# Performance work log

Measured on AMD Instinct MI355X. Metric: run time of the kernel, lower is better.

The kernel has to match this reference:

```python
import jax, jax.numpy as jnp
import numpy as np
import math

NUM_HEADS = 16
HEAD_DIM = 64
DIM = 1024
IO_SLOTS = 16
NEG_INF = 1.0e9


def _alibi_slopes(num_heads):
    # slopes = ratio**i for i in 1..n, ratio = 2**(-8/n)
    ratio = 2.0 ** (-8.0 / num_heads)
    return jnp.array([ratio ** i for i in range(1, num_heads + 1)], dtype=jnp.float32)


def setup_inputs() -> dict:
    key = jax.random.key(0)
    ks = jax.random.split(key, 7)
    B, S, D = 2, 2048, DIM
    x = jax.random.normal(ks[0], (B, S, D), dtype=jnp.float32)
    is_getchar = jax.random.uniform(ks[1], (B, S), dtype=jnp.float32)
    is_putchar = jax.random.uniform(ks[2], (B, S), dtype=jnp.float32)
    scale = 0.02
    wq = jax.random.normal(ks[3], (D, NUM_HEADS * HEAD_DIM), dtype=jnp.float32) * scale
    wk = jax.random.normal(ks[4], (D, NUM_HEADS * HEAD_DIM), dtype=jnp.float32) * scale
    wv = jax.random.normal(ks[5], (D, NUM_HEADS * HEAD_DIM), dtype=jnp.float32) * scale
    wo = jax.random.normal(ks[6], (NUM_HEADS * HEAD_DIM, D), dtype=jnp.float32) * scale
    return {"x": x, "is_getchar": is_getchar, "is_putchar": is_putchar,
            "wq": wq, "wk": wk, "wv": wv, "wo": wo}


def reference(x, is_getchar, is_putchar, wq, wk, wv, wo):
    B, S, D = x.shape
    H, hd = NUM_HEADS, HEAD_DIM
    io_start = D - IO_SLOTS

    q = (x @ wq).reshape(B, S, H, hd)
    k = (x @ wk).reshape(B, S, H, hd)
    v = (x @ wv).reshape(B, S, H, hd)

    # scores[b,h,i,j] = q . k / sqrt(hd)
    scores = jnp.einsum("bihd,bjhd->bhij", q, k) / math.sqrt(hd)

    # standard ALiBi bias: -slope * (i - j), causal masked
    positions = jnp.arange(S)
    dist = (positions[:, None] - positions[None, :]).astype(jnp.float32)  # [S,S] = i - j
    slopes = _alibi_slopes(H)  # [H]
    bias = -slopes[:, None, None] * dist  # [H,S,S]
    causal = jnp.triu(jnp.ones((S, S), dtype=jnp.float32), k=1)
    bias = bias - causal * NEG_INF
    scores = scores + bias[None]

    # targeted read-head bias on head 0: -slope0 * |target - j|
    read_anchor = x[..., io_start + 0]  # [B,S]
    read_offset = x[..., io_start + 1]  # [B,S]
    target = read_anchor + 1.0 + read_offset  # [B,S]
    read_bias = -slopes[0] * jnp.abs(target[..., None] - positions.astype(jnp.float32))  # [B,S,S]
    head0 = jnp.where(is_getchar[:, None, :, None] > 0.5, read_bias[:, None], scores[:, :1])
    scores = scores.at[:, :1].set(head0)

    attn = jax.nn.softmax(scores, axis=-1)
    attn_out = jnp.einsum("bhij,bjhd->bihd", attn, v).reshape(B, S, H * hd)
    output = x + attn_out @ wo

    # I/O state updates (last 16 channels)
    output = output.at[..., io_start + 1].add(is_getchar)   # read_offset += getchar
    output = output.at[..., io_start + 3].add(is_putchar)   # write_offset += putchar
    output = output.at[..., io_start + 13].set(is_putchar)  # output_ready = putchar
    return output
```

## Files before the change

kernel.cpp:

```cpp
#include <hip/hip_runtime.h>
#include <hip/hip_bf16.h>

typedef __hip_bfloat16 bf16;
typedef __attribute__((ext_vector_type(8))) short short8;
typedef __attribute__((ext_vector_type(4))) short short4v;
typedef __attribute__((ext_vector_type(4))) float f32x4;

#define MFMA16(a, b, c) __builtin_amdgcn_mfma_f32_16x16x32_bf16((a), (b), (c), 0, 0, 0)

#if __has_builtin(__builtin_amdgcn_mfma_f32_16x16x16bf16_1k)
#define MFMA_PV(a, b, c) __builtin_amdgcn_mfma_f32_16x16x16bf16_1k((a), (b), (c), 0, 0, 0)
#elif __has_builtin(__builtin_amdgcn_mfma_f32_16x16x16_bf16)
#define MFMA_PV(a, b, c) __builtin_amdgcn_mfma_f32_16x16x16_bf16((a), (b), (c), 0, 0, 0)
#else
static __device__ __forceinline__ f32x4 mfma_pv_asm(short4v a, short4v b, f32x4 c) {
    f32x4 d;
    asm volatile("v_mfma_f32_16x16x16_bf16 %0, %1, %2, %3"
                 : "=&v"(d) : "v"(a), "v"(b), "v"(c));
    return d;
}
#define MFMA_PV(a, b, c) mfma_pv_asm((a), (b), (c))
#endif

static __device__ __forceinline__ void gload_lds16(const bf16* g, bf16* l) {
    __builtin_amdgcn_global_load_lds((const __attribute__((address_space(1))) void*)g,
                                     (__attribute__((address_space(3))) void*)l, 16, 0, 0);
}

__global__ __launch_bounds__(256) void cast_x_kernel(const float* __restrict__ in,
                                                     bf16* __restrict__ out) {
    int i = (blockIdx.x * 256 + threadIdx.x) * 4;
    float4 v = *(const float4*)(in + i);
    union { bf16 h4[4]; uint2 u; } p;
    p.h4[0] = __float2bfloat16(v.x);
    p.h4[1] = __float2bfloat16(v.y);
    p.h4[2] = __float2bfloat16(v.z);
    p.h4[3] = __float2bfloat16(v.w);
    *(uint2*)(out + i) = p.u;
}

__global__ __launch_bounds__(256) void transpose_cast_kernel(
    const float* __restrict__ wq, const float* __restrict__ wk,
    const float* __restrict__ wv, const float* __restrict__ wo,
    bf16* __restrict__ WqkvT, bf16* __restrict__ WoT) {
    __shared__ bf16 tile[64][65];
    int bid = blockIdx.x;
    int mat = bid >> 8;
    int t   = bid & 255;
    int tn  = t >> 4, tk = t & 15;
    const float* src = (mat == 0) ? wq : (mat == 1) ? wk : (mat == 2) ? wv : wo;
    bf16* dst = (mat < 3) ? (WqkvT + (size_t)mat * 1024 * 1024) : WoT;
    int tx = threadIdx.x & 63, ty = threadIdx.x >> 6;
    int k0 = tk * 64, n0 = tn * 64;
#pragma unroll
    for (int p = 0; p < 16; ++p) {
        int r = p * 4 + ty;
        tile[r][tx] = __float2bfloat16(src[(size_t)(k0 + r) * 1024 + n0 + tx]);
    }
    __syncthreads();
#pragma unroll
    for (int p = 0; p < 16; ++p) {
        int r = p * 4 + ty;
        dst[(size_t)(n0 + r) * 1024 + k0 + tx] = tile[tx][r];
    }
}

__global__ __launch_bounds__(256) void gemm_qkv_kernel(
    const bf16* __restrict__ A, const bf16* __restrict__ Bt,
    bf16* __restrict__ QK, bf16* __restrict__ Vt) {
    const int K = 1024;
    int bm = blockIdx.x, bn = blockIdx.y;
    __shared__ bf16 As[128 * 32];
    __shared__ bf16 Bs[128 * 32];
    int tid = threadIdx.x;
    int lane = tid & 63, w = tid >> 6;
    int wm = (w >> 1) * 64, wn = (w & 1) * 64;
    int q4 = lane >> 4, li = lane & 15;
    int srow = tid >> 2, sc = (tid & 3) * 8;

    const bf16* Ag = A + (size_t)(bm * 128 + srow) * K + sc;
    const bf16* Bg = Bt + (size_t)(bn * 128 + srow) * K + sc;
    bf16* Asl = As + tid * 8;
    bf16* Asl2 = As + 2048 + tid * 8;
    bf16* Bsl = Bs + tid * 8;
    bf16* Bsl2 = Bs + 2048 + tid * 8;

    f32x4 acc[4][4];
#pragma unroll
    for (int mt = 0; mt < 4; ++mt)
#pragma unroll
        for (int nt = 0; nt < 4; ++nt) acc[mt][nt] = (f32x4){0.f, 0.f, 0.f, 0.f};

    for (int k0 = 0; k0 < K; k0 += 32) {
        __syncthreads();
        gload_lds16(Ag + k0, Asl);
        gload_lds16(Ag + 64 * K + k0, Asl2);
        gload_lds16(Bg + k0, Bsl);
        gload_lds16(Bg + 64 * K + k0, Bsl2);
        __syncthreads();
        short8 af[4], bfb[4];
#pragma unroll
        for (int mt = 0; mt < 4; ++mt)
            af[mt] = *(const short8*)(As + (wm + mt * 16 + li) * 32 + q4 * 8);
#pragma unroll
        for (int nt = 0; nt < 4; ++nt)
            bfb[nt] = *(const short8*)(Bs + (wn + nt * 16 + li) * 32 + q4 * 8);
#pragma unroll
        for (int mt = 0; mt < 4; ++mt)
#pragma unroll
            for (int nt = 0; nt < 4; ++nt)
                acc[mt][nt] = MFMA16(af[mt], bfb[nt], acc[mt][nt]);
    }

    int rowb = bm * 128 + wm;
    if (bn < 16) {
#pragma unroll
        for (int mt = 0; mt < 4; ++mt) {
#pragma unroll
            for (int nt = 0; nt < 4; ++nt) {
                int col = bn * 128 + wn + nt * 16 + li;
#pragma unroll
                for (int r = 0; r < 4; ++r) {
                    int row = rowb + mt * 16 + q4 * 4 + r;
                    QK[(size_t)row * 2048 + col] = __float2bfloat16(acc[mt][nt][r]);
                }
            }
        }
    } else {
#pragma unroll
        for (int mt = 0; mt < 4; ++mt) {
            int sbase = rowb + mt * 16 + q4 * 4;
            int b = sbase >> 11, s = sbase & 2047;
#pragma unroll
            for (int nt = 0; nt < 4; ++nt) {
                int n = bn * 128 + wn + nt * 16 + li - 2048;
                int h = n >> 6, d = n & 63;
                union { bf16 h4[4]; uint2 u; } pk;
#pragma unroll
                for (int r = 0; r < 4; ++r) pk.h4[r] = __float2bfloat16(acc[mt][nt][r]);
                *(uint2*)(Vt + (size_t)((b * 16 + h) * 64 + d) * 2048 + s) = pk.u;
            }
        }
    }
}

__global__ __launch_bounds__(256, 3) void attn_kernel(
    const bf16* __restrict__ QK, const bf16* __restrict__ Vt,
    const float* __restrict__ x, const float* __restrict__ gch,
    bf16* __restrict__ AO) {
    const int S = 2048;
    int idx = blockIdx.x;
    int ti, h, b;
    if (idx < 64) { h = 0; b = idx & 1; ti = idx >> 1; }
    else {
        int i2 = idx - 64;
        int row = i2 / 30;
        int j = i2 - row * 30;
        ti = 31 - row; h = 1 + (j >> 1); b = j & 1;
    }
    int i0 = ti * 64;
    int tid = threadIdx.x, lane = tid & 63, w = tid >> 6;
    int q4 = lane >> 4, li = lane & 15;

    __shared__ bf16 Ks[64 * 72];
    __shared__ bf16 Vs[64 * 72];
    __shared__ float Ored[64 * 68];
    __shared__ float lsumBuf[4][64];

    short8 qf[4][2];
#pragma unroll
    for (int it = 0; it < 4; ++it) {
        const bf16* qp = QK + (size_t)(b * S + i0 + it * 16 + li) * 2048 + h * 64 + q4 * 8;
        qf[it][0] = *(const short8*)(qp);
        qf[it][1] = *(const short8*)(qp + 32);
    }

    const float L2E = 1.4426950408889634f;
    float slope = exp2f(-0.5f * (float)(h + 1));
    float s1  = 0.125f * L2E;
    float sl1 = slope * L2E;
    const float slope0_1 = 0.70710678118654752f * L2E;

    float tgt[4]; int gcm[4];
    if (h == 0) {
#pragma unroll
        for (int it = 0; it < 4; ++it) {
            size_t ix = (size_t)(b * S + i0 + it * 16 + li);
            gcm[it] = gch[ix] > 0.5f ? 1 : 0;
            tgt[it] = x[ix * 1024 + 1008] + 1.0f + x[ix * 1024 + 1009];
        }
    } else {
#pragma unroll
        for (int it = 0; it < 4; ++it) { gcm[it] = 0; tgt[it] = 0.f; }
    }

    float lsum[4] = {0.f, 0.f, 0.f, 0.f};
    f32x4 o[4][4];
#pragma unroll
    for (int it = 0; it < 4; ++it)
#pragma unroll
        for (int dt = 0; dt < 4; ++dt) o[it][dt] = (f32x4){0.f, 0.f, 0.f, 0.f};

    int srow = tid >> 3, scv = (tid & 7) * 8;
    const bf16* Kg = QK + (size_t)(b * S + srow) * 2048 + 1024 + h * 64 + scv;
    const bf16* Vg = Vt + (size_t)((b * 16 + h) * 64 + srow) * 2048 + scv;

    int ntiles = (h == 0) ? (S / 64) : (ti + 1);
    for (int jt = 0; jt < ntiles; ++jt) {
        int j0 = jt * 64;
        uint4 kv0 = *(const uint4*)(Kg + (size_t)j0 * 2048);
        uint4 kv1 = *(const uint4*)(Kg + (size_t)(j0 + 32) * 2048);
        uint4 vv0 = *(const uint4*)(Vg + j0);
        uint4 vv1 = *(const uint4*)(Vg + (size_t)32 * 2048 + j0);
        __syncthreads();
        *(uint4*)(Ks + srow * 72 + scv) = kv0;
        *(uint4*)(Ks + (srow + 32) * 72 + scv) = kv1;
        *(uint4*)(Vs + srow * 72 + scv) = vv0;
        *(uint4*)(Vs + (srow + 32) * 72 + scv) = vv1;
        __syncthreads();

        short8 kf0 = *(const short8*)(Ks + (w * 16 + li) * 72 + q4 * 8);
        short8 kf1 = *(const short8*)(Ks + (w * 16 + li) * 72 + 32 + q4 * 8);
        f32x4 sAcc[4];
#pragma unroll
        for (int it = 0; it < 4; ++it) {
            f32x4 z = (f32x4){0.f, 0.f, 0.f, 0.f};
            z = MFMA16(kf0, qf[it][0], z);
            z = MFMA16(kf1, qf[it][1], z);
            sAcc[it] = z;
        }

        float jbase = (float)(j0 + w * 16 + q4 * 4);
        int maskable = (jt >= ti);
        short4v pf[4];
#pragma unroll
        for (int it = 0; it < 4; ++it) {
            float fi = (float)(i0 + it * 16 + li);
            float d0 = jbase - fi;
            union { bf16 hh[4]; short4v v; } pu;
#pragma unroll
            for (int r = 0; r < 4; ++r) {
                float dj = d0 + (float)r;
                float s = fmaf(sl1, dj, sAcc[it][r] * s1);
                float p;
                if (h == 0) {
                    float jj = jbase + (float)r;
                    float sg = -slope0_1 * fabsf(tgt[it] - jj);
                    s = gcm[it] ? sg : s;
                    bool msk = (!gcm[it]) && (dj > 0.f);
                    p = msk ? 0.f : exp2f(s);
                } else {
                    p = exp2f(s);
                    if (maskable && dj > 0.f) p = 0.f;
                }
                lsum[it] += p;
                pu.hh[r] = __float2bfloat16(p);
            }
            pf[it] = pu.v;
        }

#pragma unroll
        for (int dt = 0; dt < 4; ++dt) {
            short4v vf = *(const short4v*)(Vs + (dt * 16 + li) * 72 + w * 16 + q4 * 4);
#pragma unroll
            for (int it = 0; it < 4; ++it)
                o[it][dt] = MFMA_PV(pf[it], vf, o[it][dt]);
        }
    }

#pragma unroll
    for (int it = 0; it < 4; ++it) {
        lsum[it] += __shfl_xor(lsum[it], 16, 64);
        lsum[it] += __shfl_xor(lsum[it], 32, 64);
    }
    if (lane < 16) {
#pragma unroll
        for (int it = 0; it < 4; ++it) lsumBuf[w][it * 16 + lane] = lsum[it];
    }

    __syncthreads();
    if (w == 0) {
#pragma unroll
        for (int it = 0; it < 4; ++it)
#pragma unroll
            for (int dt = 0; dt < 4; ++dt)
#pragma unroll
                for (int r = 0; r < 4; ++r)
                    Ored[(it * 16 + q4 * 4 + r) * 68 + dt * 16 + li] = o[it][dt][r];
    }
    __syncthreads();
    if (w == 1) {
#pragma unroll
        for (int it = 0; it < 4; ++it)
#pragma unroll
            for (int dt = 0; dt < 4; ++dt)
#pragma unroll
                for (int r = 0; r < 4; ++r)
                    Ored[(it * 16 + q4 * 4 + r) * 68 + dt * 16 + li] += o[it][dt][r];
    }
    __syncthreads();
    if (w == 2) {
#pragma unroll
        for (int it = 0; it < 4; ++it)
#pragma unroll
            for (int dt = 0; dt < 4; ++dt)
#pragma unroll
                for (int r = 0; r < 4; ++r)
                    Ored[(it * 16 + q4 * 4 + r) * 68 + dt * 16 + li] += o[it][dt][r];
    }
    __syncthreads();
    if (w == 3) {
#pragma unroll
        for (int it = 0; it < 4; ++it)
#pragma unroll
            for (int dt = 0; dt < 4; ++dt)
#pragma unroll
                for (int r = 0; r < 4; ++r)
                    Ored[(it * 16 + q4 * 4 + r) * 68 + dt * 16 + li] += o[it][dt][r];
    }
    __syncthreads();

    int i = tid >> 2, dseg = (tid & 3) * 16;
    float ls = lsumBuf[0][i] + lsumBuf[1][i] + lsumBuf[2][i] + lsumBuf[3][i];
    float inv = 1.0f / ls;
    bf16* dst = AO + (size_t)(b * S + i0 + i) * 1024 + h * 64 + dseg;
    union { bf16 hh[16]; uint4 u[2]; } ou;
#pragma unroll
    for (int c = 0; c < 16; ++c)
        ou.hh[c] = __float2bfloat16(Ored[i * 68 + dseg + c] * inv);
    *(uint4*)(dst) = ou.u[0];
    *(uint4*)(dst + 8) = ou.u[1];
}

__global__ __launch_bounds__(256) void gemm_out_kernel(
    const bf16* __restrict__ A, const bf16* __restrict__ Bt,
    const float* __restrict__ x, float* __restrict__ out) {
    const int K = 1024;
    int bm = blockIdx.x, bn = blockIdx.y;
    __shared__ bf16 As[128 * 32];
    __shared__ bf16 Bs[128 * 32];
    int tid = threadIdx.x;
    int lane = tid & 63, w = tid >> 6;
    int wm = (w >> 1) * 64, wn = (w & 1) * 64;
    int q4 = lane >> 4, li = lane & 15;
    int srow = tid >> 2, sc = (tid & 3) * 8;

    const bf16* Ag = A + (size_t)(bm * 128 + srow) * K + sc;
    const bf16* Bg = Bt + (size_t)(bn * 128 + srow) * K + sc;
    bf16* Asl = As + tid * 8;
    bf16* Asl2 = As + 2048 + tid * 8;
    bf16* Bsl = Bs + tid * 8;
    bf16* Bsl2 = Bs + 2048 + tid * 8;

    f32x4 acc[4][4];
#pragma unroll
    for (int mt = 0; mt < 4; ++mt)
#pragma unroll
        for (int nt = 0; nt < 4; ++nt) acc[mt][nt] = (f32x4){0.f, 0.f, 0.f, 0.f};

    for (int k0 = 0; k0 < K; k0 += 32) {
        __syncthreads();
        gload_lds16(Ag + k0, Asl);
        gload_lds16(Ag + 64 * K + k0, Asl2);
        gload_lds16(Bg + k0, Bsl);
        gload_lds16(Bg + 64 * K + k0, Bsl2);
        __syncthreads();
        short8 af[4], bfb[4];
#pragma unroll
        for (int mt = 0; mt < 4; ++mt)
            af[mt] = *(const short8*)(As + (wm + mt * 16 + li) * 32 + q4 * 8);
#pragma unroll
        for (int nt = 0; nt < 4; ++nt)
            bfb[nt] = *(const short8*)(Bs + (wn + nt * 16 + li) * 32 + q4 * 8);
#pragma unroll
        for (int mt = 0; mt < 4; ++mt)
#pragma unroll
            for (int nt = 0; nt < 4; ++nt)
                acc[mt][nt] = MFMA16(af[mt], bfb[nt], acc[mt][nt]);
    }

#pragma unroll
    for (int mt = 0; mt < 4; ++mt) {
#pragma unroll
        for (int nt = 0; nt < 4; ++nt) {
            int col = bn * 128 + wn + nt * 16 + li;
#pragma unroll
            for (int r = 0; r < 4; ++r) {
                int row = bm * 128 + wm + mt * 16 + q4 * 4 + r;
                size_t idx = (size_t)row * 1024 + col;
                out[idx] = x[idx] + acc[mt][nt][r];
            }
        }
    }
}

__global__ __launch_bounds__(256) void io_fix_kernel(float* __restrict__ out,
                                                     const float* __restrict__ gch,
                                                     const float* __restrict__ pch) {
    int r = blockIdx.x * 256 + threadIdx.x;
    float g = gch[r], p = pch[r];
    size_t base = (size_t)r * 1024;
    out[base + 1009] += g;
    out[base + 1011] += p;
    out[base + 1021] = p;
}

extern "C" void kernel_launch(void* const* d_in, const int* in_sizes, int n_in,
                              void* d_out, int out_size, void* d_ws, size_t ws_size,
                              hipStream_t stream) {
    (void)in_sizes; (void)n_in; (void)out_size; (void)ws_size;
    const float* x   = (const float*)d_in[0];
    const float* gch = (const float*)d_in[1];
    const float* pch = (const float*)d_in[2];
    const float* wq  = (const float*)d_in[3];
    const float* wk  = (const float*)d_in[4];
    const float* wv  = (const float*)d_in[5];
    const float* wo  = (const float*)d_in[6];
    float* out = (float*)d_out;

    char* ws = (char*)d_ws;
    bf16* Xb    = (bf16*)(ws);
    bf16* WqkvT = (bf16*)(ws + (size_t)( 8 << 20));
    bf16* WoT   = (bf16*)(ws + (size_t)(14 << 20));
    bf16* QK    = (bf16*)(ws + (size_t)(16 << 20));
    bf16* Vt    = (bf16*)(ws + (size_t)(32 << 20));
    bf16* AO    = Xb;

    cast_x_kernel<<<4096, 256, 0, stream>>>(x, Xb);
    transpose_cast_kernel<<<1024, 256, 0, stream>>>(wq, wk, wv, wo, WqkvT, WoT);
    gemm_qkv_kernel<<<dim3(32, 24), 256, 0, stream>>>(Xb, WqkvT, QK, Vt);
    attn_kernel<<<1024, 256, 0, stream>>>(QK, Vt, x, gch, AO);
    gemm_out_kernel<<<dim3(32, 8), 256, 0, stream>>>(AO, WoT, x, out);
    io_fix_kernel<<<16, 256, 0, stream>>>(out, gch, pch);
}
```

Measured before the change: 207.9 us.

## Give each attention wave its own query rows, double-buffer K/V, fuse IO fixups

The attention kernel now gives each wave 16 query rows across all 64 keys, instead of splitting keys across waves. This removes the LDS cross-wave reduction of partial outputs and its chain of barriers. K/V tiles are double-buffered in shared memory with register prefetch two tiles ahead, the 1/sqrt(d)*log2e scale is folded into Q at the QKV GEMM epilogue, and occupancy is raised to 4 blocks per CU. The io_fix kernel is folded into the output GEMM epilogue to save a launch. The cost is that each wave now reads more K/V from LDS, and folding the scale into Q before the bf16 rounding changes rounding slightly.

```diff
diff --git a/kernel.cpp b/kernel.cpp
--- a/kernel.cpp
+++ b/kernel.cpp
@@ -114,6 +114,7 @@
 
     int rowb = bm * 128 + wm;
     if (bn < 16) {
+        float qs = (bn < 8) ? 0.1803368801111244f : 1.0f;
 #pragma unroll
         for (int mt = 0; mt < 4; ++mt) {
 #pragma unroll
@@ -122,7 +123,7 @@
 #pragma unroll
                 for (int r = 0; r < 4; ++r) {
                     int row = rowb + mt * 16 + q4 * 4 + r;
-                    QK[(size_t)row * 2048 + col] = __float2bfloat16(acc[mt][nt][r]);
+                    QK[(size_t)row * 2048 + col] = __float2bfloat16(acc[mt][nt][r] * qs);
                 }
             }
         }
@@ -144,7 +145,7 @@
     }
 }
 
-__global__ __launch_bounds__(256, 3) void attn_kernel(
+__global__ __launch_bounds__(256, 4) void attn_kernel(
     const bf16* __restrict__ QK, const bf16* __restrict__ Vt,
     const float* __restrict__ x, const float* __restrict__ gch,
     bf16* __restrict__ AO) {
@@ -162,179 +163,140 @@
     int tid = threadIdx.x, lane = tid & 63, w = tid >> 6;
     int q4 = lane >> 4, li = lane & 15;
 
-    __shared__ bf16 Ks[64 * 72];
-    __shared__ bf16 Vs[64 * 72];
-    __shared__ float Ored[64 * 68];
-    __shared__ float lsumBuf[4][64];
-
-    short8 qf[4][2];
-#pragma unroll
-    for (int it = 0; it < 4; ++it) {
-        const bf16* qp = QK + (size_t)(b * S + i0 + it * 16 + li) * 2048 + h * 64 + q4 * 8;
-        qf[it][0] = *(const short8*)(qp);
-        qf[it][1] = *(const short8*)(qp + 32);
-    }
+    __shared__ bf16 Ks[2][64 * 72];
+    __shared__ bf16 Vs[2][64 * 72];
+
+    int iG = i0 + w * 16 + li;
+
+    const bf16* qp = QK + (size_t)(b * S + iG) * 2048 + h * 64 + q4 * 8;
+    short8 qf0 = *(const short8*)(qp);
+    short8 qf1 = *(const short8*)(qp + 32);
 
     const float L2E = 1.4426950408889634f;
-    float slope = exp2f(-0.5f * (float)(h + 1));
-    float s1  = 0.125f * L2E;
-    float sl1 = slope * L2E;
-    const float slope0_1 = 0.70710678118654752f * L2E;
-
-    float tgt[4]; int gcm[4];
+    float sl1 = exp2f(-0.5f * (float)(h + 1)) * L2E;
+    const float slope0L = 0.70710678118654752f * L2E;
+
+    float tgj = 0.f; bool gcm = false;
     if (h == 0) {
-#pragma unroll
-        for (int it = 0; it < 4; ++it) {
-            size_t ix = (size_t)(b * S + i0 + it * 16 + li);
-            gcm[it] = gch[ix] > 0.5f ? 1 : 0;
-            tgt[it] = x[ix * 1024 + 1008] + 1.0f + x[ix * 1024 + 1009];
-        }
-    } else {
-#pragma unroll
-        for (int it = 0; it < 4; ++it) { gcm[it] = 0; tgt[it] = 0.f; }
-    }
-
-    float lsum[4] = {0.f, 0.f, 0.f, 0.f};
-    f32x4 o[4][4];
-#pragma unroll
-    for (int it = 0; it < 4; ++it)
-#pragma unroll
-        for (int dt = 0; dt < 4; ++dt) o[it][dt] = (f32x4){0.f, 0.f, 0.f, 0.f};
+        size_t ix = (size_t)(b * S + iG);
+        gcm = gch[ix] > 0.5f;
+        tgj = x[ix * 1024 + 1008] + 1.0f + x[ix * 1024 + 1009] - (float)iG;
+    }
+
+    float lsum = 0.f;
+    f32x4 o[4];
+#pragma unroll
+    for (int dt = 0; dt < 4; ++dt) o[dt] = (f32x4){0.f, 0.f, 0.f, 0.f};
 
     int srow = tid >> 3, scv = (tid & 7) * 8;
     const bf16* Kg = QK + (size_t)(b * S + srow) * 2048 + 1024 + h * 64 + scv;
     const bf16* Vg = Vt + (size_t)((b * 16 + h) * 64 + srow) * 2048 + scv;
 
     int ntiles = (h == 0) ? (S / 64) : (ti + 1);
+
+    uint4 kv0 = *(const uint4*)(Kg);
+    uint4 kv1 = *(const uint4*)(Kg + (size_t)32 * 2048);
+    uint4 vv0 = *(const uint4*)(Vg);
+    uint4 vv1 = *(const uint4*)(Vg + (size_t)32 * 2048);
+    *(uint4*)(Ks[0] + srow * 72 + scv) = kv0;
+    *(uint4*)(Ks[0] + (srow + 32) * 72 + scv) = kv1;
+    *(uint4*)(Vs[0] + srow * 72 + scv) = vv0;
+    *(uint4*)(Vs[0] + (srow + 32) * 72 + scv) = vv1;
+    if (ntiles > 1) {
+        kv0 = *(const uint4*)(Kg + (size_t)64 * 2048);
+        kv1 = *(const uint4*)(Kg + (size_t)96 * 2048);
+        vv0 = *(const uint4*)(Vg + 64);
+        vv1 = *(const uint4*)(Vg + (size_t)32 * 2048 + 64);
+    }
+    __syncthreads();
+
     for (int jt = 0; jt < ntiles; ++jt) {
+        const bf16* KsB = Ks[jt & 1];
+        const bf16* VsB = Vs[jt & 1];
+        if (jt + 1 < ntiles) {
+            bf16* Kn = Ks[(jt + 1) & 1];
+            bf16* Vn = Vs[(jt + 1) & 1];
+            *(uint4*)(Kn + srow * 72 + scv) = kv0;
+            *(uint4*)(Kn + (srow + 32) * 72 + scv) = kv1;
+            *(uint4*)(Vn + srow * 72 + scv) = vv0;
+            *(uint4*)(Vn + (srow + 32) * 72 + scv) = vv1;
+            if (jt + 2 < ntiles) {
+                size_t jn = (size_t)(jt + 2) * 64;
+                kv0 = *(const uint4*)(Kg + jn * 2048);
+                kv1 = *(const uint4*)(Kg + (jn + 32) * 2048);
+                vv0 = *(const uint4*)(Vg + jn);
+                vv1 = *(const uint4*)(Vg + (size_t)32 * 2048 + jn);
+            }
+        }
+
         int j0 = jt * 64;
-        uint4 kv0 = *(const uint4*)(Kg + (size_t)j0 * 2048);
-        uint4 kv1 = *(const uint4*)(Kg + (size_t)(j0 + 32) * 2048);
-        uint4 vv0 = *(const uint4*)(Vg + j0);
-        uint4 vv1 = *(const uint4*)(Vg + (size_t)32 * 2048 + j0);
-        __syncthreads();
-        *(uint4*)(Ks + srow * 72 + scv) = kv0;
-        *(uint4*)(Ks + (srow + 32) * 72 + scv) = kv1;
-        *(uint4*)(Vs + srow * 72 + scv) = vv0;
-        *(uint4*)(Vs + (srow + 32) * 72 + scv) = vv1;
-        __syncthreads();
-
-        short8 kf0 = *(const short8*)(Ks + (w * 16 + li) * 72 + q4 * 8);
-        short8 kf1 = *(const short8*)(Ks + (w * 16 + li) * 72 + 32 + q4 * 8);
-        f32x4 sAcc[4];
-#pragma unroll
-        for (int it = 0; it < 4; ++it) {
+        f32x4 sA[4];
+#pragma unroll
+        for (int nt = 0; nt < 4; ++nt) {
+            short8 kf0 = *(const short8*)(KsB + (nt * 16 + li) * 72 + q4 * 8);
+            short8 kf1 = *(const short8*)(KsB + (nt * 16 + li) * 72 + 32 + q4 * 8);
             f32x4 z = (f32x4){0.f, 0.f, 0.f, 0.f};
-            z = MFMA16(kf0, qf[it][0], z);
-            z = MFMA16(kf1, qf[it][1], z);
-            sAcc[it] = z;
-        }
-
-        float jbase = (float)(j0 + w * 16 + q4 * 4);
-        int maskable = (jt >= ti);
-        short4v pf[4];
-#pragma unroll
-        for (int it = 0; it < 4; ++it) {
-            float fi = (float)(i0 + it * 16 + li);
-            float d0 = jbase - fi;
+            z = MFMA16(kf0, qf0, z);
+            z = MFMA16(kf1, qf1, z);
+            sA[nt] = z;
+        }
+
+        bool diag = (jt >= ti);
+        short4v pB[4];
+#pragma unroll
+        for (int nt = 0; nt < 4; ++nt) {
+            float djb = (float)(j0 + nt * 16 + q4 * 4 - iG);
             union { bf16 hh[4]; short4v v; } pu;
 #pragma unroll
             for (int r = 0; r < 4; ++r) {
-                float dj = d0 + (float)r;
-                float s = fmaf(sl1, dj, sAcc[it][r] * s1);
+                float dj = djb + (float)r;
                 float p;
                 if (h == 0) {
-                    float jj = jbase + (float)r;
-                    float sg = -slope0_1 * fabsf(tgt[it] - jj);
-                    s = gcm[it] ? sg : s;
-                    bool msk = (!gcm[it]) && (dj > 0.f);
-                    p = msk ? 0.f : exp2f(s);
+                    float s = fmaf(sl1, dj, sA[nt][r]);
+                    float sg = -slope0L * fabsf(tgj - dj);
+                    s = gcm ? sg : s;
+                    p = exp2f(s);
+                    if (!gcm && dj > 0.f) p = 0.f;
                 } else {
+                    float s = fmaf(sl1, dj, sA[nt][r]);
                     p = exp2f(s);
-                    if (maskable && dj > 0.f) p = 0.f;
+                    if (diag && dj > 0.f) p = 0.f;
                 }
-                lsum[it] += p;
+                lsum += p;
                 pu.hh[r] = __float2bfloat16(p);
             }
-            pf[it] = pu.v;
-        }
-
-#pragma unroll
-        for (int dt = 0; dt < 4; ++dt) {
-            short4v vf = *(const short4v*)(Vs + (dt * 16 + li) * 72 + w * 16 + q4 * 4);
-#pragma unroll
-            for (int it = 0; it < 4; ++it)
-                o[it][dt] = MFMA_PV(pf[it], vf, o[it][dt]);
-        }
-    }
-
-#pragma unroll
-    for (int it = 0; it < 4; ++it) {
-        lsum[it] += __shfl_xor(lsum[it], 16, 64);
-        lsum[it] += __shfl_xor(lsum[it], 32, 64);
-    }
-    if (lane < 16) {
-#pragma unroll
-        for (int it = 0; it < 4; ++it) lsumBuf[w][it * 16 + lane] = lsum[it];
-    }
-
-    __syncthreads();
-    if (w == 0) {
-#pragma unroll
-        for (int it = 0; it < 4; ++it)
-#pragma unroll
-            for (int dt = 0; dt < 4; ++dt)
-#pragma unroll
-                for (int r = 0; r < 4; ++r)
-                    Ored[(it * 16 + q4 * 4 + r) * 68 + dt * 16 + li] = o[it][dt][r];
-    }
-    __syncthreads();
-    if (w == 1) {
-#pragma unroll
-        for (int it = 0; it < 4; ++it)
-#pragma unroll
-            for (int dt = 0; dt < 4; ++dt)
-#pragma unroll
-                for (int r = 0; r < 4; ++r)
-                    Ored[(it * 16 + q4 * 4 + r) * 68 + dt * 16 + li] += o[it][dt][r];
-    }
-    __syncthreads();
-    if (w == 2) {
-#pragma unroll
-        for (int it = 0; it < 4; ++it)
-#pragma unroll
-            for (int dt = 0; dt < 4; ++dt)
-#pragma unroll
-                for (int r = 0; r < 4; ++r)
-                    Ored[(it * 16 + q4 * 4 + r) * 68 + dt * 16 + li] += o[it][dt][r];
-    }
-    __syncthreads();
-    if (w == 3) {
-#pragma unroll
-        for (int it = 0; it < 4; ++it)
-#pragma unroll
-            for (int dt = 0; dt < 4; ++dt)
-#pragma unroll
-                for (int r = 0; r < 4; ++r)
-                    Ored[(it * 16 + q4 * 4 + r) * 68 + dt * 16 + li] += o[it][dt][r];
-    }
-    __syncthreads();
-
-    int i = tid >> 2, dseg = (tid & 3) * 16;
-    float ls = lsumBuf[0][i] + lsumBuf[1][i] + lsumBuf[2][i] + lsumBuf[3][i];
-    float inv = 1.0f / ls;
-    bf16* dst = AO + (size_t)(b * S + i0 + i) * 1024 + h * 64 + dseg;
-    union { bf16 hh[16]; uint4 u[2]; } ou;
-#pragma unroll
-    for (int c = 0; c < 16; ++c)
-        ou.hh[c] = __float2bfloat16(Ored[i * 68 + dseg + c] * inv);
-    *(uint4*)(dst) = ou.u[0];
-    *(uint4*)(dst + 8) = ou.u[1];
+            pB[nt] = pu.v;
+        }
+
+#pragma unroll
+        for (int nt = 0; nt < 4; ++nt) {
+#pragma unroll
+            for (int dt = 0; dt < 4; ++dt) {
+                short4v vf = *(const short4v*)(VsB + (dt * 16 + li) * 72 + nt * 16 + q4 * 4);
+                o[dt] = MFMA_PV(vf, pB[nt], o[dt]);
+            }
+        }
+        __syncthreads();
+    }
+
+    lsum += __shfl_xor(lsum, 16, 64);
+    lsum += __shfl_xor(lsum, 32, 64);
+    float inv = 1.0f / lsum;
+
+    bf16* dst = AO + (size_t)(b * S + iG) * 1024 + h * 64 + q4 * 4;
+#pragma unroll
+    for (int dt = 0; dt < 4; ++dt) {
+        union { bf16 h4[4]; uint2 u; } ou;
+#pragma unroll
+        for (int r = 0; r < 4; ++r) ou.h4[r] = __float2bfloat16(o[dt][r] * inv);
+        *(uint2*)(dst + dt * 16) = ou.u;
+    }
 }
 
 __global__ __launch_bounds__(256) void gemm_out_kernel(
     const bf16* __restrict__ A, const bf16* __restrict__ Bt,
-    const float* __restrict__ x, float* __restrict__ out) {
+    const float* __restrict__ x, const float* __restrict__ gch,
+    const float* __restrict__ pch, float* __restrict__ out) {
     const int K = 1024;
     int bm = blockIdx.x, bn = blockIdx.y;
     __shared__ bf16 As[128 * 32];
@@ -388,21 +350,14 @@
             for (int r = 0; r < 4; ++r) {
                 int row = bm * 128 + wm + mt * 16 + q4 * 4 + r;
                 size_t idx = (size_t)row * 1024 + col;
-                out[idx] = x[idx] + acc[mt][nt][r];
-            }
-        }
-    }
-}
-
-__global__ __launch_bounds__(256) void io_fix_kernel(float* __restrict__ out,
-                                                     const float* __restrict__ gch,
-                                                     const float* __restrict__ pch) {
-    int r = blockIdx.x * 256 + threadIdx.x;
-    float g = gch[r], p = pch[r];
-    size_t base = (size_t)r * 1024;
-    out[base + 1009] += g;
-    out[base + 1011] += p;
-    out[base + 1021] = p;
+                float v = x[idx] + acc[mt][nt][r];
+                if (col == 1009) v += gch[row];
+                else if (col == 1011) v += pch[row];
+                else if (col == 1021) v = pch[row];
+                out[idx] = v;
+            }
+        }
+    }
 }
 
 extern "C" void kernel_launch(void* const* d_in, const int* in_sizes, int n_in,
@@ -430,6 +385,5 @@
     transpose_cast_kernel<<<1024, 256, 0, stream>>>(wq, wk, wv, wo, WqkvT, WoT);
     gemm_qkv_kernel<<<dim3(32, 24), 256, 0, stream>>>(Xb, WqkvT, QK, Vt);
     attn_kernel<<<1024, 256, 0, stream>>>(QK, Vt, x, gch, AO);
-    gemm_out_kernel<<<dim3(32, 8), 256, 0, stream>>>(AO, WoT, x, out);
-    io_fix_kernel<<<16, 256, 0, stream>>>(out, gch, pch);
-}
+    gemm_out_kernel<<<dim3(32, 8), 256, 0, stream>>>(AO, WoT, x, gch, pch, out);
+}
```

New measurement: 214.1 us. 3.0% more time.
